# Kernel optimization log

Hardware: AMD Instinct MI355X
Metric: run time of the kernel (lower is better)

The kernel has to match this reference:

```python
import jax, jax.numpy as jnp
import numpy as np

C_IN = 128
C_QK = C_IN // 8


def setup_inputs() -> dict:
    key = jax.random.key(0)
    kx, kq, kk, kv = jax.random.split(key, 4)
    x = jax.random.normal(kx, (8, C_IN, 64, 64), dtype=jnp.float32)
    # 1x1 conv weights, stored as (c_out, c_in); fan-in scaled init
    s = 1.0 / np.sqrt(C_IN)
    Wq = jax.random.normal(kq, (C_QK, C_IN), dtype=jnp.float32) * s
    Wk = jax.random.normal(kk, (C_QK, C_IN), dtype=jnp.float32) * s
    Wv = jax.random.normal(kv, (C_IN, C_IN), dtype=jnp.float32) * s
    gamma = jnp.ones((1,), dtype=jnp.float32) * 0.5  # nonzero so residual branch matters
    return {"x": x, "Wq": Wq, "Wk": Wk, "Wv": Wv, "gamma": gamma}


def reference(x, Wq, Wk, Wv, gamma):
    b, c, h, w = x.shape
    xt = rearr = x.reshape(b, c, h * w)            # b c n
    q = jnp.einsum('oc,bcn->bno', Wq, xt)          # b n c//8
    k = jnp.einsum('oc,bcn->bon', Wk, xt)          # b c//8 n
    v = jnp.einsum('oc,bcn->bno', Wv, xt)          # b n c
    energy = jnp.einsum('bno,bom->bnm', q, k)      # b n n (no scale, per source)
    attn = jax.nn.softmax(energy, axis=-1)
    out = jnp.einsum('bnm,bmc->bnc', attn, v)      # b n c
    out = out.transpose(0, 2, 1).reshape(b, c, h, w)
    return x + gamma[0] * out
```

## Files before the change

### kernel.cpp

```cpp
#include <hip/hip_runtime.h>
#include <hip/hip_bf16.h>


typedef __bf16 bf16x8 __attribute__((ext_vector_type(8)));
typedef __bf16 bf16x4 __attribute__((ext_vector_type(4)));
typedef float  f32x16 __attribute__((ext_vector_type(16)));

static constexpr int Bb = 8, Cc = 128, Nn = 4096, CQ = 16;

__device__ __forceinline__ f32x16 mfma32(bf16x8 a, bf16x8 b, f32x16 c) {
    return __builtin_amdgcn_mfma_f32_32x32x16_bf16(a, b, c, 0, 0, 0);
}
struct HL { __bf16 h, l; };
__device__ __forceinline__ HL hilo(float f) {
    HL r;
    r.h = (__bf16)f;
    r.l = (__bf16)(f - (float)r.h);
    return r;
}
__device__ __forceinline__ unsigned int pack2bf(float a, float b) {
    union { __bf16 h[2]; unsigned int u; } x;
    x.h[0] = (__bf16)a; x.h[1] = (__bf16)b;
    return x.u;
}

__global__ __launch_bounds__(256) void qkv_kernel(
    const float* __restrict__ x, const float* __restrict__ Wq,
    const float* __restrict__ Wk, const float* __restrict__ Wv,
    __bf16* __restrict__ qw, __bf16* __restrict__ kw, __bf16* __restrict__ vw)
{
    const int b = blockIdx.y, n0 = blockIdx.x * 64, t = threadIdx.x;
    const int wave = t >> 6, lane = t & 63, lr = lane & 31, lq = lane >> 5;

    __shared__ __bf16 xh[64][136], xl[64][136];
    __shared__ __bf16 wqh[32][136], wql[32][136];
    __shared__ __bf16 wvh[128][136];

    {
        const int n = t & 63, ug = t >> 6;
        #pragma unroll
        for (int i = 0; i < 4; ++i) {
            const int ci0 = (ug * 4 + i) * 8;
            float v[8];
            #pragma unroll
            for (int k = 0; k < 8; ++k)
                v[k] = x[((size_t)(b * Cc + ci0 + k)) * Nn + n0 + n];
            bf16x8 h8, l8;
            #pragma unroll
            for (int k = 0; k < 8; ++k) { HL z = hilo(v[k]); h8[k] = z.h; l8[k] = z.l; }
            *(bf16x8*)&xh[n][ci0] = h8;
            *(bf16x8*)&xl[n][ci0] = l8;
        }
    }
    #pragma unroll
    for (int i = 0; i < 8; ++i) {
        int idx = t + i * 256;
        int o = idx >> 7, ci = idx & 127;
        HL zq = hilo(Wq[idx]);
        wqh[o][ci] = zq.h; wql[o][ci] = zq.l;
        HL zk = hilo(Wk[idx]);
        wqh[16 + o][ci] = zk.h; wql[16 + o][ci] = zk.l;
    }
    #pragma unroll
    for (int i = 0; i < 16; ++i) {
        int flat = t * 4 + i * 1024;
        float4 w4 = *(const float4*)(Wv + flat);
        int c = flat >> 7, ci0 = flat & 127;
        bf16x4 h4 = { (__bf16)w4.x, (__bf16)w4.y, (__bf16)w4.z, (__bf16)w4.w };
        *(bf16x4*)&wvh[c][ci0] = h4;
    }
    __syncthreads();

    if (wave < 2) {
        const int nh = wave;
        f32x16 acc = {};
        #pragma unroll
        for (int ks = 0; ks < 8; ++ks) {
            bf16x8 ah = *(const bf16x8*)&wqh[lr][ks * 16 + lq * 8];
            bf16x8 al = *(const bf16x8*)&wql[lr][ks * 16 + lq * 8];
            bf16x8 bh = *(const bf16x8*)&xh[nh * 32 + lr][ks * 16 + lq * 8];
            bf16x8 bl = *(const bf16x8*)&xl[nh * 32 + lr][ks * 16 + lq * 8];
            acc = mfma32(ah, bh, acc);
            acc = mfma32(al, bh, acc);
            acc = mfma32(ah, bl, acc);
        }
        const int tile = (n0 >> 5) + nh;
        __bf16* qb = qw + (((size_t)b * 128 + tile) << 10);
        __bf16* kb = kw + (((size_t)b * 128 + tile) << 10);
        #pragma unroll
        for (int r = 0; r < 16; ++r) {
            int op = (r & 3) + 8 * (r >> 2) + 4 * lq;
            if (op < 16) {
                HL z = hilo(acc[r] * 1.44269504089f);
                int off = (op >> 3) * 256 + lr * 8 + (op & 7);
                qb[off] = z.h; qb[512 + off] = z.l;
            } else {
                int ch = op - 16;
                HL z = hilo(acc[r]);
                int off = (ch >> 3) * 256 + lr * 8 + (ch & 7);
                kb[off] = z.h; kb[512 + off] = z.l;
            }
        }
    }
    {
        int tl[3][2]; int nt;
        if      (wave == 0) { tl[0][0]=2; tl[0][1]=0; nt=1; }
        else if (wave == 1) { tl[0][0]=2; tl[0][1]=1; nt=1; }
        else if (wave == 2) { tl[0][0]=0; tl[0][1]=0; tl[1][0]=1; tl[1][1]=0; tl[2][0]=3; tl[2][1]=0; nt=3; }
        else                { tl[0][0]=0; tl[0][1]=1; tl[1][0]=1; tl[1][1]=1; tl[2][0]=3; tl[2][1]=1; nt=3; }
        const int fK = (lr >> 4) & 1, lqK = (lr >> 3) & 1, jK = lr & 7;
        const int lof = fK * 512 + lqK * 256 + jK;
        for (int ti = 0; ti < nt; ++ti) {
            const int ct = tl[ti][0], nh = tl[ti][1];
            f32x16 acc = {};
            #pragma unroll
            for (int ks = 0; ks < 8; ++ks) {
                bf16x8 a  = *(const bf16x8*)&wvh[ct * 32 + lr][ks * 16 + lq * 8];
                bf16x8 bh = *(const bf16x8*)&xh[nh * 32 + lr][ks * 16 + lq * 8];
                acc = mfma32(a, bh, acc);
            }
            const int chunk = (n0 >> 5) + nh;
            __bf16* vb = vw + (((size_t)b * 128 + chunk) << 12);
            #pragma unroll
            for (int r = 0; r < 16; ++r) {
                int c = (r & 3) + 8 * (r >> 2) + 4 * lq + ct * 32;
                vb[ct * 1024 + lof + (c & 31) * 8] = (__bf16)acc[r];
            }
        }
    }
}

__global__ __launch_bounds__(256, 3) void attn_kernel(
    const float* __restrict__ x, const __bf16* __restrict__ qw,
    const __bf16* __restrict__ kw, const __bf16* __restrict__ vw,
    const float* __restrict__ gamma, float* __restrict__ out)
{
    const int h = blockIdx.x;
    const int b = h & 7;
    const int qt = h >> 3;
    const int t = threadIdx.x;
    const int wave = t >> 6, lane = t & 63, lr = lane & 31, lq = lane >> 5;

    __shared__ float accbuf[32][129];
    __shared__ float lbuf[32];

    const __bf16* qb = qw + (((size_t)b * 128 + qt) << 10) + lane * 8;
    const bf16x8 qhi = *(const bf16x8*)qb;
    const bf16x8 qlo = *(const bf16x8*)(qb + 512);

    const __bf16* kwb = kw + (((size_t)b * 128) << 10);
    const __bf16* vwb = vw + (((size_t)b * 128) << 12);
    const int c0 = wave * 32;

    bf16x8 khi, klo;
    {
        const __bf16* kp = kwb + ((size_t)c0 << 10) + lane * 8;
        khi = *(const bf16x8*)kp;
        klo = *(const bf16x8*)(kp + 512);
    }

    f32x16 acc[4] = {{}, {}, {}, {}};
    float l_part = 0.f;

    for (int it = 0; it < 32; ++it) {
        const __bf16* vp = vwb + ((size_t)(c0 + it) << 12) + lane * 8;
        bf16x8 vf[8];
        #pragma unroll
        for (int u = 0; u < 8; ++u) vf[u] = *(const bf16x8*)(vp + u * 512);

        bf16x8 nkh, nkl;
        {
            const int nc = c0 + (it < 31 ? it + 1 : it);
            const __bf16* kp = kwb + ((size_t)nc << 10) + lane * 8;
            nkh = *(const bf16x8*)kp;
            nkl = *(const bf16x8*)(kp + 512);
        }

        f32x16 s = {};
        s = mfma32(khi, qhi, s);
        s = mfma32(klo, qhi, s);
        s = mfma32(khi, qlo, s);

        float p[16];
        #pragma unroll
        for (int r = 0; r < 16; ++r) p[r] = __builtin_amdgcn_exp2f(s[r]);
        l_part += ((((p[0] + p[1]) + (p[2] + p[3])) + ((p[4] + p[5]) + (p[6] + p[7])))
                 + (((p[8] + p[9]) + (p[10] + p[11])) + ((p[12] + p[13]) + (p[14] + p[15]))));

        unsigned int G00 = pack2bf(p[0],  p[1]),  G01 = pack2bf(p[2],  p[3]);
        unsigned int G10 = pack2bf(p[4],  p[5]),  G11 = pack2bf(p[6],  p[7]);
        unsigned int G20 = pack2bf(p[8],  p[9]),  G21 = pack2bf(p[10], p[11]);
        unsigned int G30 = pack2bf(p[12], p[13]), G31 = pack2bf(p[14], p[15]);

        unsigned int sA0 = lq ? G00 : G10, sA1 = lq ? G01 : G11;
        unsigned int sB0 = lq ? G20 : G30, sB1 = lq ? G21 : G31;
        unsigned int rA0 = __shfl_xor(sA0, 32), rA1 = __shfl_xor(sA1, 32);
        unsigned int rB0 = __shfl_xor(sB0, 32), rB1 = __shfl_xor(sB1, 32);

        union U8 { unsigned int u[4]; bf16x8 v; };
        U8 f0, f1;
        f0.u[0] = lq ? rA0 : G00;  f0.u[1] = lq ? rA1 : G01;
        f0.u[2] = lq ? G10 : rA0;  f0.u[3] = lq ? G11 : rA1;
        f1.u[0] = lq ? rB0 : G20;  f1.u[1] = lq ? rB1 : G21;
        f1.u[2] = lq ? G30 : rB0;  f1.u[3] = lq ? G31 : rB1;

        #pragma unroll
        for (int ct = 0; ct < 4; ++ct) {
            acc[ct] = mfma32(vf[ct * 2 + 0], f0.v, acc[ct]);
            acc[ct] = mfma32(vf[ct * 2 + 1], f1.v, acc[ct]);
        }

        khi = nkh; klo = nkl;
    }

    l_part += __shfl_xor(l_part, 32);

    if (wave == 0) {
        #pragma unroll
        for (int ct = 0; ct < 4; ++ct)
            #pragma unroll
            for (int r = 0; r < 16; ++r) {
                int c = (r & 3) + 8 * (r >> 2) + 4 * lq + 32 * ct;
                accbuf[lr][c] = acc[ct][r];
            }
        if (lane < 32) lbuf[lr] = l_part;
    }
    __syncthreads();
    if (wave != 0) {
        #pragma unroll
        for (int ct = 0; ct < 4; ++ct)
            #pragma unroll
            for (int r = 0; r < 16; ++r) {
                int c = (r & 3) + 8 * (r >> 2) + 4 * lq + 32 * ct;
                atomicAdd(&accbuf[lr][c], acc[ct][r]);
            }
        if (lane < 32) atomicAdd(&lbuf[lr], l_part);
    }
    __syncthreads();

    const float g = gamma[0];
    const int q = t & 31, cg = t >> 5;
    const float linv = 1.0f / lbuf[q];
    const int n0b = qt * 32;
    #pragma unroll
    for (int i = 0; i < 16; ++i) {
        int c = cg + 8 * i;
        size_t idx = ((size_t)(b * Cc + c)) * Nn + n0b + q;
        out[idx] = x[idx] + g * accbuf[q][c] * linv;
    }
}

extern "C" void kernel_launch(void* const* d_in, const int* in_sizes, int n_in,
                              void* d_out, int out_size, void* d_ws, size_t ws_size,
                              hipStream_t stream) {
    const float* x  = (const float*)d_in[0];
    const float* Wq = (const float*)d_in[1];
    const float* Wk = (const float*)d_in[2];
    const float* Wv = (const float*)d_in[3];
    const float* gm = (const float*)d_in[4];

    __bf16* qw = (__bf16*)d_ws;
    __bf16* kw = qw + (size_t)Bb * 128 * 1024;
    __bf16* vw = kw + (size_t)Bb * 128 * 1024;

    qkv_kernel<<<dim3(Nn / 64, Bb), 256, 0, stream>>>(x, Wq, Wk, Wv, qw, kw, vw);
    attn_kernel<<<dim3(Nn / 32 * Bb), 256, 0, stream>>>(x, qw, kw, vw, gm,
                                                        (float*)d_out);
}
```

Baseline: 203.3 us.

## Split attention channels across 8 waves, use permlane32 swap, vectorize QKV stores

The attention kernel goes from 256 to 512 threads. Each wave now handles a quarter of the key range and half of the value channels, which cuts per-wave accumulators from four tiles to two to lower register pressure and add parallelism. The cross-half shuffle is replaced by permlane32_swap. In the QKV kernel, Wv is read straight from global instead of staged in LDS, Q/K stores become vectorized bf16x4, and V output is transposed through a small LDS tile so stores are coalesced. The cost is more LDS atomics in the reduction and repeated Wv global reads.

New measurement: 202.9 us. Within noise of the previous version (-0.2%).

```diff
diff --git a/kernel.cpp b/kernel.cpp
--- a/kernel.cpp
+++ b/kernel.cpp
@@ -5,6 +5,7 @@
 typedef __bf16 bf16x8 __attribute__((ext_vector_type(8)));
 typedef __bf16 bf16x4 __attribute__((ext_vector_type(4)));
 typedef float  f32x16 __attribute__((ext_vector_type(16)));
+typedef unsigned int uint32x2 __attribute__((ext_vector_type(2)));
 
 static constexpr int Bb = 8, Cc = 128, Nn = 4096, CQ = 16;
 
@@ -34,7 +35,7 @@
 
     __shared__ __bf16 xh[64][136], xl[64][136];
     __shared__ __bf16 wqh[32][136], wql[32][136];
-    __shared__ __bf16 wvh[128][136];
+    __shared__ __bf16 sc[4][32][40];
 
     {
         const int n = t & 63, ug = t >> 6;
@@ -61,14 +62,6 @@
         HL zk = hilo(Wk[idx]);
         wqh[16 + o][ci] = zk.h; wql[16 + o][ci] = zk.l;
     }
-    #pragma unroll
-    for (int i = 0; i < 16; ++i) {
-        int flat = t * 4 + i * 1024;
-        float4 w4 = *(const float4*)(Wv + flat);
-        int c = flat >> 7, ci0 = flat & 127;
-        bf16x4 h4 = { (__bf16)w4.x, (__bf16)w4.y, (__bf16)w4.z, (__bf16)w4.w };
-        *(bf16x4*)&wvh[c][ci0] = h4;
-    }
     __syncthreads();
 
     if (wave < 2) {
@@ -88,18 +81,19 @@
         __bf16* qb = qw + (((size_t)b * 128 + tile) << 10);
         __bf16* kb = kw + (((size_t)b * 128 + tile) << 10);
         #pragma unroll
-        for (int r = 0; r < 16; ++r) {
-            int op = (r & 3) + 8 * (r >> 2) + 4 * lq;
-            if (op < 16) {
-                HL z = hilo(acc[r] * 1.44269504089f);
-                int off = (op >> 3) * 256 + lr * 8 + (op & 7);
-                qb[off] = z.h; qb[512 + off] = z.l;
-            } else {
-                int ch = op - 16;
-                HL z = hilo(acc[r]);
-                int off = (ch >> 3) * 256 + lr * 8 + (ch & 7);
-                kb[off] = z.h; kb[512 + off] = z.l;
-            }
+        for (int rg = 0; rg < 4; ++rg) {
+            bf16x4 h4, l4;
+            #pragma unroll
+            for (int j = 0; j < 4; ++j) {
+                float v = acc[rg * 4 + j];
+                if (rg < 2) v *= 1.44269504089f;
+                HL z = hilo(v);
+                h4[j] = z.h; l4[j] = z.l;
+            }
+            const int off = (rg & 1) * 256 + lr * 8 + 4 * lq;
+            __bf16* base = (rg < 2) ? qb : kb;
+            *(bf16x4*)(base + off) = h4;
+            *(bf16x4*)(base + 512 + off) = l4;
         }
     }
     {
@@ -108,29 +102,36 @@
         else if (wave == 1) { tl[0][0]=2; tl[0][1]=1; nt=1; }
         else if (wave == 2) { tl[0][0]=0; tl[0][1]=0; tl[1][0]=1; tl[1][1]=0; tl[2][0]=3; tl[2][1]=0; nt=3; }
         else                { tl[0][0]=0; tl[0][1]=1; tl[1][0]=1; tl[1][1]=1; tl[2][0]=3; tl[2][1]=1; nt=3; }
-        const int fK = (lr >> 4) & 1, lqK = (lr >> 3) & 1, jK = lr & 7;
-        const int lof = fK * 512 + lqK * 256 + jK;
         for (int ti = 0; ti < nt; ++ti) {
             const int ct = tl[ti][0], nh = tl[ti][1];
             f32x16 acc = {};
             #pragma unroll
             for (int ks = 0; ks < 8; ++ks) {
-                bf16x8 a  = *(const bf16x8*)&wvh[ct * 32 + lr][ks * 16 + lq * 8];
+                const float* wp = Wv + (ct * 32 + lr) * Cc + ks * 16 + lq * 8;
+                float4 w0 = *(const float4*)wp;
+                float4 w1 = *(const float4*)(wp + 4);
+                bf16x8 a = { (__bf16)w0.x, (__bf16)w0.y, (__bf16)w0.z, (__bf16)w0.w,
+                             (__bf16)w1.x, (__bf16)w1.y, (__bf16)w1.z, (__bf16)w1.w };
                 bf16x8 bh = *(const bf16x8*)&xh[nh * 32 + lr][ks * 16 + lq * 8];
                 acc = mfma32(a, bh, acc);
             }
+            #pragma unroll
+            for (int r = 0; r < 16; ++r) {
+                int crow = (r & 3) + 8 * (r >> 2) + 4 * lq;
+                sc[wave][crow][lr] = (__bf16)acc[r];
+            }
             const int chunk = (n0 >> 5) + nh;
-            __bf16* vb = vw + (((size_t)b * 128 + chunk) << 12);
-            #pragma unroll
-            for (int r = 0; r < 16; ++r) {
-                int c = (r & 3) + 8 * (r >> 2) + 4 * lq + ct * 32;
-                vb[ct * 1024 + lof + (c & 31) * 8] = (__bf16)acc[r];
-            }
-        }
-    }
-}
-
-__global__ __launch_bounds__(256, 3) void attn_kernel(
+            __bf16* vb = vw + (((size_t)b * 128 + chunk) << 12) + ct * 1024;
+            #pragma unroll
+            for (int u = 0; u < 2; ++u) {
+                bf16x8 row = *(const bf16x8*)&sc[wave][lr][u * 16 + lq * 8];
+                *(bf16x8*)(vb + u * 512 + lane * 8) = row;
+            }
+        }
+    }
+}
+
+__global__ __launch_bounds__(512, 4) void attn_kernel(
     const float* __restrict__ x, const __bf16* __restrict__ qw,
     const __bf16* __restrict__ kw, const __bf16* __restrict__ vw,
     const float* __restrict__ gamma, float* __restrict__ out)
@@ -140,6 +141,7 @@
     const int qt = h >> 3;
     const int t = threadIdx.x;
     const int wave = t >> 6, lane = t & 63, lr = lane & 31, lq = lane >> 5;
+    const int kr = wave & 3, ch = wave >> 2;
 
     __shared__ float accbuf[32][129];
     __shared__ float lbuf[32];
@@ -149,8 +151,8 @@
     const bf16x8 qlo = *(const bf16x8*)(qb + 512);
 
     const __bf16* kwb = kw + (((size_t)b * 128) << 10);
-    const __bf16* vwb = vw + (((size_t)b * 128) << 12);
-    const int c0 = wave * 32;
+    const __bf16* vwb = vw + (((size_t)b * 128) << 12) + ch * 2048;
+    const int c0 = kr * 32;
 
     bf16x8 khi, klo;
     {
@@ -159,14 +161,15 @@
         klo = *(const bf16x8*)(kp + 512);
     }
 
-    f32x16 acc[4] = {{}, {}, {}, {}};
+    f32x16 acc0 = {}, acc1 = {};
     float l_part = 0.f;
 
     for (int it = 0; it < 32; ++it) {
         const __bf16* vp = vwb + ((size_t)(c0 + it) << 12) + lane * 8;
-        bf16x8 vf[8];
-        #pragma unroll
-        for (int u = 0; u < 8; ++u) vf[u] = *(const bf16x8*)(vp + u * 512);
+        bf16x8 vf0 = *(const bf16x8*)(vp);
+        bf16x8 vf1 = *(const bf16x8*)(vp + 512);
+        bf16x8 vf2 = *(const bf16x8*)(vp + 1024);
+        bf16x8 vf3 = *(const bf16x8*)(vp + 1536);
 
         bf16x8 nkh, nkl;
         {
@@ -192,49 +195,51 @@
         unsigned int G20 = pack2bf(p[8],  p[9]),  G21 = pack2bf(p[10], p[11]);
         unsigned int G30 = pack2bf(p[12], p[13]), G31 = pack2bf(p[14], p[15]);
 
-        unsigned int sA0 = lq ? G00 : G10, sA1 = lq ? G01 : G11;
-        unsigned int sB0 = lq ? G20 : G30, sB1 = lq ? G21 : G31;
-        unsigned int rA0 = __shfl_xor(sA0, 32), rA1 = __shfl_xor(sA1, 32);
-        unsigned int rB0 = __shfl_xor(sB0, 32), rB1 = __shfl_xor(sB1, 32);
+        {
+            uint32x2 r;
+            r = __builtin_amdgcn_permlane32_swap(G00, G10, false, false);
+            G00 = r[0]; G10 = r[1];
+            r = __builtin_amdgcn_permlane32_swap(G01, G11, false, false);
+            G01 = r[0]; G11 = r[1];
+            r = __builtin_amdgcn_permlane32_swap(G20, G30, false, false);
+            G20 = r[0]; G30 = r[1];
+            r = __builtin_amdgcn_permlane32_swap(G21, G31, false, false);
+            G21 = r[0]; G31 = r[1];
+        }
 
         union U8 { unsigned int u[4]; bf16x8 v; };
-        U8 f0, f1;
-        f0.u[0] = lq ? rA0 : G00;  f0.u[1] = lq ? rA1 : G01;
-        f0.u[2] = lq ? G10 : rA0;  f0.u[3] = lq ? G11 : rA1;
-        f1.u[0] = lq ? rB0 : G20;  f1.u[1] = lq ? rB1 : G21;
-        f1.u[2] = lq ? G30 : rB0;  f1.u[3] = lq ? G31 : rB1;
-
-        #pragma unroll
-        for (int ct = 0; ct < 4; ++ct) {
-            acc[ct] = mfma32(vf[ct * 2 + 0], f0.v, acc[ct]);
-            acc[ct] = mfma32(vf[ct * 2 + 1], f1.v, acc[ct]);
-        }
+        U8 F0, F1;
+        F0.u[0] = G00; F0.u[1] = G01; F0.u[2] = G10; F0.u[3] = G11;
+        F1.u[0] = G20; F1.u[1] = G21; F1.u[2] = G30; F1.u[3] = G31;
+
+        acc0 = mfma32(vf0, F0.v, acc0);
+        acc0 = mfma32(vf1, F1.v, acc0);
+        acc1 = mfma32(vf2, F0.v, acc1);
+        acc1 = mfma32(vf3, F1.v, acc1);
 
         khi = nkh; klo = nkl;
     }
 
     l_part += __shfl_xor(l_part, 32);
 
-    if (wave == 0) {
-        #pragma unroll
-        for (int ct = 0; ct < 4; ++ct)
-            #pragma unroll
-            for (int r = 0; r < 16; ++r) {
-                int c = (r & 3) + 8 * (r >> 2) + 4 * lq + 32 * ct;
-                accbuf[lr][c] = acc[ct][r];
-            }
-        if (lane < 32) lbuf[lr] = l_part;
+    if (kr == 0) {
+        #pragma unroll
+        for (int r = 0; r < 16; ++r) {
+            int c = ch * 64 + (r & 3) + 8 * (r >> 2) + 4 * lq;
+            accbuf[lr][c] = acc0[r];
+            accbuf[lr][c + 32] = acc1[r];
+        }
+        if (wave == 0 && lane < 32) lbuf[lr] = l_part;
     }
     __syncthreads();
-    if (wave != 0) {
-        #pragma unroll
-        for (int ct = 0; ct < 4; ++ct)
-            #pragma unroll
-            for (int r = 0; r < 16; ++r) {
-                int c = (r & 3) + 8 * (r >> 2) + 4 * lq + 32 * ct;
-                atomicAdd(&accbuf[lr][c], acc[ct][r]);
-            }
-        if (lane < 32) atomicAdd(&lbuf[lr], l_part);
+    if (kr != 0) {
+        #pragma unroll
+        for (int r = 0; r < 16; ++r) {
+            int c = ch * 64 + (r & 3) + 8 * (r >> 2) + 4 * lq;
+            atomicAdd(&accbuf[lr][c], acc0[r]);
+            atomicAdd(&accbuf[lr][c + 32], acc1[r]);
+        }
+        if (ch == 0 && lane < 32) atomicAdd(&lbuf[lr], l_part);
     }
     __syncthreads();
 
@@ -243,8 +248,8 @@
     const float linv = 1.0f / lbuf[q];
     const int n0b = qt * 32;
     #pragma unroll
-    for (int i = 0; i < 16; ++i) {
-        int c = cg + 8 * i;
+    for (int i = 0; i < 8; ++i) {
+        int c = cg + 16 * i;
         size_t idx = ((size_t)(b * Cc + c)) * Nn + n0b + q;
         out[idx] = x[idx] + g * accbuf[q][c] * linv;
     }
@@ -264,6 +269,6 @@
     __bf16* vw = kw + (size_t)Bb * 128 * 1024;
 
     qkv_kernel<<<dim3(Nn / 64, Bb), 256, 0, stream>>>(x, Wq, Wk, Wv, qw, kw, vw);
-    attn_kernel<<<dim3(Nn / 32 * Bb), 256, 0, stream>>>(x, qw, kw, vw, gm,
+    attn_kernel<<<dim3(Nn / 32 * Bb), 512, 0, stream>>>(x, qw, kw, vw, gm,
                                                         (float*)d_out);
 }
```
